# Kernel optimization log

Measured on AMD Instinct MI355X. Metric: run time of the kernel, lower is better.

Reference implementation:

```python
import jax, jax.numpy as jnp
import numpy as np

N = 100000   # nodes
E = 1600000  # edges
H = 64       # hidden_dim
NT = 512     # num_taxo
TD = 32      # taxo_dim
ID = 32      # item_dim
L = 2        # taxo_layers
ETA = 0.5
SLOPE = 0.01  # leaky_relu default


def setup_inputs() -> dict:
    key = jax.random.key(0)
    ks = jax.random.split(key, 20)
    p = lambda i, shape, s: jax.random.normal(ks[i], shape, dtype=jnp.float32) * s
    return {
        'h': p(0, (N, H), 1.0),
        'src': jax.random.randint(ks[1], (E,), 0, N),
        'dst': jax.random.randint(ks[2], (E,), 0, N),
        'taxo_cats': jax.random.randint(ks[3], (N, L), 0, NT),
        'idx_rows': jnp.arange(N),
        'idx_cols': jax.random.randint(ks[4], (N,), 0, N),
        'idx_vals': jax.random.uniform(ks[5], (N,), dtype=jnp.float32),
        'norm_rows': jnp.arange(N),
        'norm_cols': jax.random.randint(ks[6], (N,), 0, N),
        'norm_vals': jax.random.uniform(ks[7], (N,), dtype=jnp.float32),
        'W_w': p(8, (H, H), H ** -0.5),
        'W_b': jnp.zeros((H,), jnp.float32),
        'prelu_a': jnp.full((1,), 0.25, jnp.float32),
        'taxo_mean': p(9, (NT, H), 0.1),
        'taxo_std_log': p(10, (NT, H), 0.1),
        'conv_wh': p(11, (1, 2 * H), (2 * H) ** -0.5),
        'conv_Ww': p(12, (H, H), H ** -0.5),
        'conv_Wb': jnp.zeros((H,), jnp.float32),
        'psi_W': p(13, (1, H, H), H ** -0.5),
        'psi_b': jnp.zeros((1,), jnp.float32),
        'mlp_w0': p(14, (TD, H), H ** -0.5),
        'mlp_b0': jnp.zeros((TD,), jnp.float32),
        'mlp_w1': p(15, (TD, H), H ** -0.5),
        'mlp_b1': jnp.zeros((TD,), jnp.float32),
        'mlp_w2': p(16, (ID, H), H ** -0.5),
        'mlp_b2': jnp.zeros((ID,), jnp.float32),
    }


def _spmm(rows, cols, vals, x, nrows):
    # sparse COO [nrows, n] @ dense [n, d]
    return jax.ops.segment_sum(vals[:, None] * x[cols], rows, num_segments=nrows)


def _edge_softmax(scores, dst, n):
    # softmax of edge scores grouped by destination node
    m = jax.ops.segment_max(scores, dst, num_segments=n)
    e = jnp.exp(scores - m[dst])
    s = jax.ops.segment_sum(e, dst, num_segments=n)
    return e / s[dst]


def _prelu(x, a):
    return jnp.where(x >= 0, x, a * x)


def _normalize(x):
    return x / jnp.maximum(jnp.linalg.norm(x, axis=1, keepdims=True), 1e-12)


def _conv(h, tax, src, dst, wh, Ww, Wb):
    hs = h[src]  # [E,H]
    wf = jnp.concatenate([hs, h[dst]], axis=1) @ wh.T  # [E,1]
    wf = jnp.where(wf >= 0, wf, SLOPE * wf)
    alpha_f = _edge_softmax(wf, dst, N)
    wt = jnp.sum(tax[src] * tax[dst], axis=1, keepdims=True)  # [E,1]
    alpha_t = _edge_softmax(wt, dst, N)
    alpha = ETA * alpha_f + (1.0 - ETA) * alpha_t
    z = jax.ops.segment_sum(hs * alpha, dst, num_segments=N)  # u_mul_e + sum
    return z @ Ww.T + Wb


def reference(h, src, dst, taxo_cats, idx_rows, idx_cols, idx_vals,
              norm_rows, norm_cols, norm_vals, W_w, W_b, prelu_a,
              taxo_mean, taxo_std_log, conv_wh, conv_Ww, conv_Wb,
              psi_W, psi_b, mlp_w0, mlp_b0, mlp_w1, mlp_b1, mlp_w2, mlp_b2):
    h = _prelu(h @ W_w.T + W_b, prelu_a)
    means = taxo_mean[taxo_cats]            # [N,L,H]
    stds = jnp.exp(taxo_std_log[taxo_cats])  # [N,L,H]
    tax = _spmm(norm_rows, norm_cols, norm_vals, means.reshape(N, L * H), N)
    # conv layers share the SAME weights (ModuleList([ConvLayer]*num_layer))
    for i in range(2):
        h = _conv(h, tax, src, dst, conv_wh, conv_Ww, conv_Wb)
        if i < 1:
            h = _prelu(h, prelu_a)
    raw = h
    emb_h = _normalize(h @ mlp_w2.T + mlp_b2)
    embs = []
    for i, (w, b) in enumerate([(mlp_w0, mlp_b0), (mlp_w1, mlp_b1)]):
        h_rev = _spmm(idx_rows, idx_cols, idx_vals, h, N)
        mi = means[:, i]
        si = stds[:, i]
        stpl = jnp.einsum('bi,ij,bj->b', h_rev, psi_W[0], mi)[:, None] + psi_b
        tau = jax.nn.sigmoid(stpl) * jnp.exp(-si)
        cur = (1.0 - tau) * h_rev + tau * mi
        cur = _spmm(norm_rows, norm_cols, norm_vals, cur, N)
        embs.append(_normalize(cur @ w.T + b))
    emb = jnp.stack(embs, axis=2).reshape(N, -1)
    emb = jnp.concatenate([emb_h, emb], axis=1)  # [N, out_dim]
    return raw, emb
```

## Files before the change

kernel.cpp:

```cpp
#include <hip/hip_runtime.h>

constexpr int H  = 64;
constexpr int NT = 512;
constexpr int NBMAX = 512;

#define FMA4(acc_, s_, v_) { (acc_).x += (s_)*(v_).x; (acc_).y += (s_)*(v_).y; \
                             (acc_).z += (s_)*(v_).z; (acc_).w += (s_)*(v_).w; }

__global__ void k_gram(const float* __restrict__ tm, float* __restrict__ G) {
    int idx = blockIdx.x * blockDim.x + threadIdx.x;
    if (idx >= NT * NT) return;
    int a = idx >> 9, b = idx & (NT - 1);
    const float* ra = tm + a * H;
    const float* rb = tm + b * H;
    float s = 0.f;
#pragma unroll
    for (int k = 0; k < H; ++k) s += ra[k] * rb[k];
    G[idx] = s;
}

__global__ void k_nm(const int* __restrict__ ncols, const int* __restrict__ cats,
                     const float* __restrict__ nvals, uint2* __restrict__ nm, int N) {
    int n = blockIdx.x * blockDim.x + threadIdx.x;
    if (n >= N) return;
    int j = ncols[n];
    nm[n] = make_uint2(__float_as_uint(nvals[n]),
                       (unsigned)(cats[j * 2] | (cats[j * 2 + 1] << 16)));
}

__global__ void k_phist(const int* __restrict__ dst, int* __restrict__ histT,
                        int NB, int NPB, int CH, int E) {
    __shared__ int hist[NBMAX];
    int b = blockIdx.x, t = threadIdx.x;
    for (int i = t; i < NB; i += 256) hist[i] = 0;
    __syncthreads();
    int e0 = b * CH, e1 = min(E, e0 + CH);
    for (int e = e0 + t; e < e1; e += 256)
        atomicAdd(&hist[dst[e] >> 8], 1);
    __syncthreads();
    for (int i = t; i < NB; i += 256) histT[i * NPB + b] = hist[i];
}

__global__ void k_btot(const int* __restrict__ histT, int* __restrict__ tot, int NPB) {
    __shared__ int sh[256];
    int bk = blockIdx.x, t = threadIdx.x;
    int s = 0;
    for (int j = t; j < NPB; j += 256) s += histT[bk * NPB + j];
    sh[t] = s;
    __syncthreads();
    for (int o = 128; o; o >>= 1) { if (t < o) sh[t] += sh[t + o]; __syncthreads(); }
    if (!t) tot[bk] = sh[0];
}

__global__ void k_bscan(const int* __restrict__ tot, int* __restrict__ bbase,
                        int* __restrict__ row_start, int NB, int N, int E) {
    __shared__ int sh[NBMAX];
    int t = threadIdx.x;
    int v = (t < NB) ? tot[t] : 0;
    sh[t] = v;
    __syncthreads();
    for (int o = 1; o < NBMAX; o <<= 1) {
        int x = (t >= o) ? sh[t - o] : 0;
        __syncthreads();
        sh[t] += x;
        __syncthreads();
    }
    if (t < NB) bbase[t] = sh[t] - v;
    if (t == 0) { bbase[NB] = E; row_start[N] = E; }
}

__global__ void k_boff(const int* __restrict__ histT, const int* __restrict__ bbase,
                       int* __restrict__ boff, int NPB) {
    __shared__ int sh[NBMAX];
    int bk = blockIdx.x, t = threadIdx.x;
    int v = (t < NPB) ? histT[bk * NPB + t] : 0;
    sh[t] = v;
    __syncthreads();
    for (int o = 1; o < NBMAX; o <<= 1) {
        int x = (t >= o) ? sh[t - o] : 0;
        __syncthreads();
        sh[t] += x;
        __syncthreads();
    }
    if (t < NPB) boff[bk * NPB + t] = bbase[bk] + sh[t] - v;
}

__global__ void k_part(const int* __restrict__ src, const int* __restrict__ dst,
                       const int* __restrict__ boff, unsigned* __restrict__ brec,
                       int NB, int NPB, int CH, int E) {
    __shared__ int cur[NBMAX];
    int b = blockIdx.x, t = threadIdx.x;
    for (int i = t; i < NB; i += 256) cur[i] = boff[i * NPB + b];
    __syncthreads();
    int e0 = b * CH, e1 = min(E, e0 + CH);
    for (int e = e0 + t; e < e1; e += 256) {
        int s = src[e], d = dst[e];
        int pos = atomicAdd(&cur[d >> 8], 1);
        brec[pos] = (unsigned)s | ((unsigned)(d & 255) << 24);
    }
}

__global__ void k_csr(const unsigned* __restrict__ brec, const int* __restrict__ bbase,
                      const uint2* __restrict__ nm, const float* __restrict__ G,
                      int* __restrict__ row_start, int* __restrict__ src_s,
                      float* __restrict__ et, float* __restrict__ sumt, int N) {
    __shared__ int   sdeg[256];
    __shared__ int   scur[256];
    __shared__ float ssum[256];
    __shared__ float snv[256];
    __shared__ int   scc[256];
    int b = blockIdx.x, t = threadIdx.x;
    int node0 = b << 8;
    int ebase = bbase[b], eend = bbase[b + 1];
    sdeg[t] = 0; scur[t] = 0; ssum[t] = 0.f;
    int n = node0 + t;
    if (n < N) { uint2 m = nm[n]; snv[t] = __uint_as_float(m.x); scc[t] = (int)m.y; }
    __syncthreads();
    for (int i = ebase + t; i < eend; i += 256)
        atomicAdd(&sdeg[brec[i] >> 24], 1);
    __syncthreads();
    int val = sdeg[t];
    for (int o = 1; o < 256; o <<= 1) {
        int x = (t >= o) ? sdeg[t - o] : 0;
        __syncthreads();
        sdeg[t] += x;
        __syncthreads();
    }
    int gstart = ebase + sdeg[t] - val;
    if (n < N) row_start[n] = gstart;
    sdeg[t] = gstart;
    __syncthreads();
    for (int i = ebase + t; i < eend; i += 256) {
        unsigned r = brec[i];
        int s = (int)(r & 0xFFFFFFu);
        int j = (int)(r >> 24);
        int c = atomicAdd(&scur[j], 1);
        int k = sdeg[j] + c;
        src_s[k] = s;
        uint2 ms = nm[s];
        float nvs = __uint_as_float(ms.x);
        int cs = (int)ms.y;
        int cd = scc[j];
        float wt = nvs * snv[j] *
                   (G[(cs & 0xffff) * NT + (cd & 0xffff)] + G[(cs >> 16) * NT + (cd >> 16)]);
        float ev = __expf(wt);
        et[k] = ev;
        atomicAdd(&ssum[j], ev);
    }
    __syncthreads();
    if (n < N) sumt[n] = ssum[t];
}

__global__ void k_agg(const float* __restrict__ h_in, const int* __restrict__ src_s,
                      const int* __restrict__ row_start, const float* __restrict__ et,
                      const float* __restrict__ sumt, const float* __restrict__ s_u,
                      const float* __restrict__ s_v, float* __restrict__ z_out, int N) {
    int t = threadIdx.x;
    int sg = t >> 4, l16 = t & 15, f = l16 * 4;
    int n = blockIdx.x * 16 + sg;
    if (n >= N) return;
    int kb = row_start[n], ke = row_start[n + 1];
    float4 z = make_float4(0.f, 0.f, 0.f, 0.f);
    if (ke > kb) {
        float sv = s_v[n];
        float ss = 0.f;
        for (int k = kb + l16; k < ke; k += 16) {
            float w = s_u[src_s[k]] + sv;
            w = w >= 0.f ? w : 0.01f * w;
            ss += __expf(w);
        }
        ss += __shfl_xor(ss, 1); ss += __shfl_xor(ss, 2);
        ss += __shfl_xor(ss, 4); ss += __shfl_xor(ss, 8);
        float invf = 0.5f / ss;
        float invt = 0.5f / sumt[n];
        int kl = ke - 1;
        float4 z0 = make_float4(0.f, 0.f, 0.f, 0.f);
        float4 z1 = z0, z2 = z0, z3 = z0;
        for (int k0 = kb; k0 < ke; k0 += 4) {
            int kB = min(k0 + 1, kl), kC = min(k0 + 2, kl), kD = min(k0 + 3, kl);
            int sA = src_s[k0], sB = src_s[kB], sC = src_s[kC], sD = src_s[kD];
            float wA = s_u[sA] + sv; wA = wA >= 0.f ? wA : 0.01f * wA;
            float wB = s_u[sB] + sv; wB = wB >= 0.f ? wB : 0.01f * wB;
            float wC = s_u[sC] + sv; wC = wC >= 0.f ? wC : 0.01f * wC;
            float wD = s_u[sD] + sv; wD = wD >= 0.f ? wD : 0.01f * wD;
            float aA = __expf(wA) * invf + et[k0] * invt;
            float aB = (k0 + 1 <= kl) ? (__expf(wB) * invf + et[kB] * invt) : 0.f;
            float aC = (k0 + 2 <= kl) ? (__expf(wC) * invf + et[kC] * invt) : 0.f;
            float aD = (k0 + 3 <= kl) ? (__expf(wD) * invf + et[kD] * invt) : 0.f;
            const float4 hA = *reinterpret_cast<const float4*>(h_in + (size_t)sA * H + f);
            const float4 hB = *reinterpret_cast<const float4*>(h_in + (size_t)sB * H + f);
            const float4 hC = *reinterpret_cast<const float4*>(h_in + (size_t)sC * H + f);
            const float4 hD = *reinterpret_cast<const float4*>(h_in + (size_t)sD * H + f);
            FMA4(z0, aA, hA); FMA4(z1, aB, hB); FMA4(z2, aC, hC); FMA4(z3, aD, hD);
        }
        z.x = (z0.x + z1.x) + (z2.x + z3.x);
        z.y = (z0.y + z1.y) + (z2.y + z3.y);
        z.z = (z0.z + z1.z) + (z2.z + z3.z);
        z.w = (z0.w + z1.w) + (z2.w + z3.w);
    }
    *reinterpret_cast<float4*>(z_out + (size_t)n * H + f) = z;
}

template <bool PRELU, bool SUV, bool EMBH>
__global__ void __launch_bounds__(256, 4)
k_trans(const float* __restrict__ in, const float* __restrict__ W,
        const float* __restrict__ b, const float* __restrict__ a_ptr,
        const float* __restrict__ wh,
        float* __restrict__ s_u_o, float* __restrict__ s_v_o,
        const float* __restrict__ w2, const float* __restrict__ b2,
        float* __restrict__ emb_out,
        float* __restrict__ out, int N) {
    __shared__ float WF[64 * 68];
    __shared__ float W2T[EMBH ? 64 * 36 : 1];
    __shared__ float xs[4][8][68];
    int t = threadIdx.x;
    for (int i = t; i < 64 * 64; i += 256) { int j = i >> 6, l = i & 63; WF[l * 68 + j] = W[i]; }
    if constexpr (EMBH) {
        for (int i = t; i < 64 * 32; i += 256) { int j = i >> 6, l = i & 63; W2T[l * 36 + j] = w2[i]; }
    }
    __syncthreads();
    int wid = t >> 6, lane = t & 63;
    int g = lane >> 4, f = lane & 15;
    float a = PRELU ? a_ptr[0] : 0.f;
    float4 bias = *reinterpret_cast<const float4*>(b + 4 * f);
    int n0 = blockIdx.x * 32 + wid * 8 + g;
    int n1 = n0 + 4;
    float4 xv0 = make_float4(0.f, 0.f, 0.f, 0.f), xv1 = xv0;
    if (n0 < N) xv0 = *reinterpret_cast<const float4*>(in + (size_t)n0 * H + 4 * f);
    if (n1 < N) xv1 = *reinterpret_cast<const float4*>(in + (size_t)n1 * H + 4 * f);
    *reinterpret_cast<float4*>(&xs[wid][g][4 * f])     = xv0;
    *reinterpret_cast<float4*>(&xs[wid][4 + g][4 * f]) = xv1;
    float4 accP = make_float4(0.f, 0.f, 0.f, 0.f), accQ = accP;
#pragma unroll 2
    for (int l0 = 0; l0 < 64; l0 += 4) {
        const float* wp = &WF[l0 * 68 + 4 * f];
        float4 wv0 = *reinterpret_cast<const float4*>(wp);
        float4 wv1 = *reinterpret_cast<const float4*>(wp + 68);
        float4 wv2 = *reinterpret_cast<const float4*>(wp + 136);
        float4 wv3 = *reinterpret_cast<const float4*>(wp + 204);
        float4 xP = *reinterpret_cast<const float4*>(&xs[wid][g][l0]);
        float4 xQ = *reinterpret_cast<const float4*>(&xs[wid][4 + g][l0]);
        FMA4(accP, xP.x, wv0); FMA4(accP, xP.y, wv1);
        FMA4(accP, xP.z, wv2); FMA4(accP, xP.w, wv3);
        FMA4(accQ, xQ.x, wv0); FMA4(accQ, xQ.y, wv1);
        FMA4(accQ, xQ.z, wv2); FMA4(accQ, xQ.w, wv3);
    }
    auto epi = [&](float4 acc, int n, int slot) {
        acc.x += bias.x; acc.y += bias.y; acc.z += bias.z; acc.w += bias.w;
        if constexpr (PRELU) {
            acc.x = acc.x >= 0.f ? acc.x : a * acc.x;
            acc.y = acc.y >= 0.f ? acc.y : a * acc.y;
            acc.z = acc.z >= 0.f ? acc.z : a * acc.z;
            acc.w = acc.w >= 0.f ? acc.w : a * acc.w;
        }
        if (n < N) *reinterpret_cast<float4*>(out + (size_t)n * H + 4 * f) = acc;
        if constexpr (SUV) {
            float4 wu = *reinterpret_cast<const float4*>(wh + 4 * f);
            float4 wv = *reinterpret_cast<const float4*>(wh + H + 4 * f);
            float u = acc.x * wu.x + acc.y * wu.y + acc.z * wu.z + acc.w * wu.w;
            float v = acc.x * wv.x + acc.y * wv.y + acc.z * wv.z + acc.w * wv.w;
            u += __shfl_xor(u, 1); v += __shfl_xor(v, 1);
            u += __shfl_xor(u, 2); v += __shfl_xor(v, 2);
            u += __shfl_xor(u, 4); v += __shfl_xor(v, 4);
            u += __shfl_xor(u, 8); v += __shfl_xor(v, 8);
            if (f == 0 && n < N) { s_u_o[n] = u; s_v_o[n] = v; }
        }
        if constexpr (EMBH) {
            *reinterpret_cast<float4*>(&xs[wid][slot][4 * f]) = acc;
            if (f < 8) {
                float4 e4 = *reinterpret_cast<const float4*>(b2 + 4 * f);
#pragma unroll 4
                for (int l0 = 0; l0 < 64; l0 += 4) {
                    float4 x4 = *reinterpret_cast<const float4*>(&xs[wid][slot][l0]);
                    float4 u0 = *reinterpret_cast<const float4*>(&W2T[(l0 + 0) * 36 + 4 * f]);
                    float4 u1 = *reinterpret_cast<const float4*>(&W2T[(l0 + 1) * 36 + 4 * f]);
                    float4 u2 = *reinterpret_cast<const float4*>(&W2T[(l0 + 2) * 36 + 4 * f]);
                    float4 u3 = *reinterpret_cast<const float4*>(&W2T[(l0 + 3) * 36 + 4 * f]);
                    FMA4(e4, x4.x, u0); FMA4(e4, x4.y, u1);
                    FMA4(e4, x4.z, u2); FMA4(e4, x4.w, u3);
                }
                float sq = e4.x * e4.x + e4.y * e4.y + e4.z * e4.z + e4.w * e4.w;
                sq += __shfl_xor(sq, 1);
                sq += __shfl_xor(sq, 2);
                sq += __shfl_xor(sq, 4);
                float invn = 1.f / fmaxf(sqrtf(sq), 1e-12f);
                e4.x *= invn; e4.y *= invn; e4.z *= invn; e4.w *= invn;
                if (n < N) *reinterpret_cast<float4*>(emb_out + (size_t)n * 96 + 4 * f) = e4;
            }
        }
    };
    epi(accP, n0, g);
    epi(accQ, n1, 4 + g);
}

__global__ void __launch_bounds__(256, 4)
k_post1(const float* __restrict__ raw, const int* __restrict__ icols,
        const float* __restrict__ ivals, const float* __restrict__ Psi,
        const float* __restrict__ psib, const int* __restrict__ cats,
        const float* __restrict__ tm, const float* __restrict__ tsl,
        float* __restrict__ cur0, float* __restrict__ cur1, int N) {
    __shared__ float PF[64 * 68];
    __shared__ float xs[4][8][68];
    int t = threadIdx.x;
    for (int i = t; i < 64 * 64; i += 256) { int l = i >> 6, j = i & 63; PF[l * 68 + j] = Psi[i]; }
    __syncthreads();
    int wid = t >> 6, lane = t & 63;
    int g = lane >> 4, f = lane & 15;
    float pb = psib[0];
    int n0 = blockIdx.x * 32 + wid * 8 + g;
    int n1 = n0 + 4;
    float4 hr0 = make_float4(0.f, 0.f, 0.f, 0.f), hr1 = hr0;
    if (n0 < N) {
        int c = icols[n0]; float iv = ivals[n0];
        float4 rv = *reinterpret_cast<const float4*>(raw + (size_t)c * H + 4 * f);
        hr0.x = iv * rv.x; hr0.y = iv * rv.y; hr0.z = iv * rv.z; hr0.w = iv * rv.w;
    }
    if (n1 < N) {
        int c = icols[n1]; float iv = ivals[n1];
        float4 rv = *reinterpret_cast<const float4*>(raw + (size_t)c * H + 4 * f);
        hr1.x = iv * rv.x; hr1.y = iv * rv.y; hr1.z = iv * rv.z; hr1.w = iv * rv.w;
    }
    *reinterpret_cast<float4*>(&xs[wid][g][4 * f])     = hr0;
    *reinterpret_cast<float4*>(&xs[wid][4 + g][4 * f]) = hr1;
    float4 v0 = make_float4(0.f, 0.f, 0.f, 0.f), v1 = v0;
#pragma unroll 2
    for (int l0 = 0; l0 < 64; l0 += 4) {
        const float* pp = &PF[l0 * 68 + 4 * f];
        float4 pv0 = *reinterpret_cast<const float4*>(pp);
        float4 pv1 = *reinterpret_cast<const float4*>(pp + 68);
        float4 pv2 = *reinterpret_cast<const float4*>(pp + 136);
        float4 pv3 = *reinterpret_cast<const float4*>(pp + 204);
        float4 xP = *reinterpret_cast<const float4*>(&xs[wid][g][l0]);
        float4 xQ = *reinterpret_cast<const float4*>(&xs[wid][4 + g][l0]);
        FMA4(v0, xP.x, pv0); FMA4(v0, xP.y, pv1); FMA4(v0, xP.z, pv2); FMA4(v0, xP.w, pv3);
        FMA4(v1, xQ.x, pv0); FMA4(v1, xQ.y, pv1); FMA4(v1, xQ.z, pv2); FMA4(v1, xQ.w, pv3);
    }
    auto epi = [&](float4 v, float4 hr, int n) {
        if (n >= N) return;
#pragma unroll
        for (int i2 = 0; i2 < 2; ++i2) {
            int c = cats[n * 2 + i2];
            float4 m4 = *reinterpret_cast<const float4*>(tm + (size_t)c * H + 4 * f);
            float sd = v.x * m4.x + v.y * m4.y + v.z * m4.z + v.w * m4.w;
            sd += __shfl_xor(sd, 1);
            sd += __shfl_xor(sd, 2);
            sd += __shfl_xor(sd, 4);
            sd += __shfl_xor(sd, 8);
            float sig = 1.f / (1.f + __expf(-(sd + pb)));
            float4 t4 = *reinterpret_cast<const float4*>(tsl + (size_t)c * H + 4 * f);
            float4 tau, cv;
            tau.x = sig * __expf(-__expf(t4.x));
            tau.y = sig * __expf(-__expf(t4.y));
            tau.z = sig * __expf(-__expf(t4.z));
            tau.w = sig * __expf(-__expf(t4.w));
            cv.x = (1.f - tau.x) * hr.x + tau.x * m4.x;
            cv.y = (1.f - tau.y) * hr.y + tau.y * m4.y;
            cv.z = (1.f - tau.z) * hr.z + tau.z * m4.z;
            cv.w = (1.f - tau.w) * hr.w + tau.w * m4.w;
            *reinterpret_cast<float4*>((i2 ? cur1 : cur0) + (size_t)n * H + 4 * f) = cv;
        }
    };
    epi(v0, hr0, n0);
    epi(v1, hr1, n1);
}

__global__ void __launch_bounds__(256, 4)
k_post2(const float* __restrict__ cur0, const float* __restrict__ cur1,
        const int* __restrict__ ncols, const float* __restrict__ nvals,
        const float* __restrict__ w0, const float* __restrict__ b0,
        const float* __restrict__ w1, const float* __restrict__ b1,
        float* __restrict__ emb_out, int N) {
    __shared__ float WC[64 * 68];
    __shared__ float xs[4][4][2][68];
    int t = threadIdx.x;
    for (int i = t; i < 64 * 64; i += 256) {
        int j = i >> 6, l = i & 63;
        WC[l * 68 + j] = (j < 32) ? w0[j * 64 + l] : w1[(j - 32) * 64 + l];
    }
    __syncthreads();
    int wid = t >> 6, lane = t & 63;
    int g = lane >> 4, f = lane & 15;
    int half = f >> 3;
    const float* bb = half ? b1 : b0;
    float4 bias = *reinterpret_cast<const float4*>(bb + 4 * (f & 7));
    for (int it = 0; it < 2; ++it) {
        int n = blockIdx.x * 32 + wid * 8 + it * 4 + g;
        float4 x0 = make_float4(0.f, 0.f, 0.f, 0.f), x1 = x0;
        if (n < N) {
            int c = ncols[n];
            float gsc = nvals[n];
            float4 c0v = *reinterpret_cast<const float4*>(cur0 + (size_t)c * H + 4 * f);
            float4 c1v = *reinterpret_cast<const float4*>(cur1 + (size_t)c * H + 4 * f);
            x0.x = gsc * c0v.x; x0.y = gsc * c0v.y; x0.z = gsc * c0v.z; x0.w = gsc * c0v.w;
            x1.x = gsc * c1v.x; x1.y = gsc * c1v.y; x1.z = gsc * c1v.z; x1.w = gsc * c1v.w;
        }
        *reinterpret_cast<float4*>(&xs[wid][g][0][4 * f]) = x0;
        *reinterpret_cast<float4*>(&xs[wid][g][1][4 * f]) = x1;
        float4 acc = bias;
#pragma unroll 4
        for (int l0 = 0; l0 < 64; l0 += 4) {
            float4 x4  = *reinterpret_cast<const float4*>(&xs[wid][g][half][l0]);
            float4 wv0 = *reinterpret_cast<const float4*>(&WC[(l0 + 0) * 68 + 4 * f]);
            float4 wv1 = *reinterpret_cast<const float4*>(&WC[(l0 + 1) * 68 + 4 * f]);
            float4 wv2 = *reinterpret_cast<const float4*>(&WC[(l0 + 2) * 68 + 4 * f]);
            float4 wv3 = *reinterpret_cast<const float4*>(&WC[(l0 + 3) * 68 + 4 * f]);
            FMA4(acc, x4.x, wv0); FMA4(acc, x4.y, wv1);
            FMA4(acc, x4.z, wv2); FMA4(acc, x4.w, wv3);
        }
        float sq = acc.x * acc.x + acc.y * acc.y + acc.z * acc.z + acc.w * acc.w;
        sq += __shfl_xor(sq, 1);
        sq += __shfl_xor(sq, 2);
        sq += __shfl_xor(sq, 4);
        float invn = 1.f / fmaxf(sqrtf(sq), 1e-12f);
        if (n < N) {
            int jb = (f & 7) * 4;
            float* o = emb_out + (size_t)n * 96 + 32 + half;
            o[2 * (jb + 0)] = acc.x * invn;
            o[2 * (jb + 1)] = acc.y * invn;
            o[2 * (jb + 2)] = acc.z * invn;
            o[2 * (jb + 3)] = acc.w * invn;
        }
    }
}

extern "C" void kernel_launch(void* const* d_in, const int* in_sizes, int n_in,
                              void* d_out, int out_size, void* d_ws, size_t ws_size,
                              hipStream_t stream) {
    const float* h      = (const float*)d_in[0];
    const int*   src    = (const int*)d_in[1];
    const int*   dst    = (const int*)d_in[2];
    const int*   cats   = (const int*)d_in[3];
    const int*   icols  = (const int*)d_in[5];
    const float* ivals  = (const float*)d_in[6];
    const int*   ncols  = (const int*)d_in[8];
    const float* nvals  = (const float*)d_in[9];
    const float* W_w    = (const float*)d_in[10];
    const float* W_b    = (const float*)d_in[11];
    const float* pre_a  = (const float*)d_in[12];
    const float* tm     = (const float*)d_in[13];
    const float* tsl    = (const float*)d_in[14];
    const float* wh     = (const float*)d_in[15];
    const float* cWw    = (const float*)d_in[16];
    const float* cWb    = (const float*)d_in[17];
    const float* psiW   = (const float*)d_in[18];
    const float* psib   = (const float*)d_in[19];
    const float* w0     = (const float*)d_in[20];
    const float* b0     = (const float*)d_in[21];
    const float* w1     = (const float*)d_in[22];
    const float* b1     = (const float*)d_in[23];
    const float* w2     = (const float*)d_in[24];
    const float* b2     = (const float*)d_in[25];

    const int N = in_sizes[0] / H;
    const int E = in_sizes[1];
    const int NB = (N + 255) >> 8;
    const int NPB = NB;
    const int CH = (E + NPB - 1) / NPB;

    char* ws = (char*)d_ws;
    size_t off = 0;
    auto alloc = [&](size_t bytes) -> void* {
        void* p = ws + off;
        off = (off + bytes + 255) & ~(size_t)255;
        return p;
    };
    float*    A        = (float*)   alloc((size_t)N * H * 4);
    float*    B        = (float*)   alloc((size_t)N * H * 4);
    float*    Z        = (float*)   alloc((size_t)N * H * 4);
    float*    et       = (float*)   alloc((size_t)E * 4);
    int*      src_s    = (int*)     alloc((size_t)E * 4);
    unsigned* brec     = (unsigned*)alloc((size_t)E * 4);
    uint2*    nm       = (uint2*)   alloc((size_t)N * 8);
    int*      row_start= (int*)     alloc((size_t)(N + 1) * 4);
    float*    sumt     = (float*)   alloc((size_t)N * 4);
    float*    s_u0     = (float*)   alloc((size_t)N * 4);
    float*    s_v0     = (float*)   alloc((size_t)N * 4);
    float*    s_u1     = (float*)   alloc((size_t)N * 4);
    float*    s_v1     = (float*)   alloc((size_t)N * 4);
    float*    G        = (float*)   alloc((size_t)NT * NT * 4);
    int*      histT    = (int*)     alloc((size_t)NB * NPB * 4);
    int*      boff     = (int*)     alloc((size_t)NB * NPB * 4);
    int*      tot      = (int*)     alloc((size_t)NB * 4);
    int*      bbase    = (int*)     alloc((size_t)(NB + 1) * 4);
    (void)ws_size; (void)n_in; (void)out_size;

    float* rawOut  = (float*)d_out;
    float* emb_out = (float*)d_out + (size_t)N * H;

    dim3 b256(256);
    int nb16 = (N + 15) / 16;
    int nb32 = (N + 31) / 32;

    k_gram<<<(NT * NT + 255) / 256, b256, 0, stream>>>(tm, G);
    k_nm<<<(N + 255) / 256, b256, 0, stream>>>(ncols, cats, nvals, nm, N);
    k_phist<<<NPB, b256, 0, stream>>>(dst, histT, NB, NPB, CH, E);
    k_btot<<<NB, b256, 0, stream>>>(histT, tot, NPB);
    k_bscan<<<1, NBMAX, 0, stream>>>(tot, bbase, row_start, NB, N, E);
    k_boff<<<NB, NBMAX, 0, stream>>>(histT, bbase, boff, NPB);
    k_part<<<NPB, b256, 0, stream>>>(src, dst, boff, brec, NB, NPB, CH, E);
    k_csr<<<NB, b256, 0, stream>>>(brec, bbase, nm, G, row_start, src_s, et, sumt, N);

    k_trans<true, true, false><<<nb32, b256, 0, stream>>>(
        h, W_w, W_b, pre_a, wh, s_u0, s_v0, nullptr, nullptr, nullptr, A, N);

    k_agg<<<nb16, b256, 0, stream>>>(A, src_s, row_start, et, sumt, s_u0, s_v0, Z, N);
    k_trans<true, true, false><<<nb32, b256, 0, stream>>>(
        Z, cWw, cWb, pre_a, wh, s_u1, s_v1, nullptr, nullptr, nullptr, B, N);

    k_agg<<<nb16, b256, 0, stream>>>(B, src_s, row_start, et, sumt, s_u1, s_v1, Z, N);
    k_trans<false, false, true><<<nb32, b256, 0, stream>>>(
        Z, cWw, cWb, pre_a, nullptr, nullptr, nullptr, w2, b2, emb_out, rawOut, N);

    k_post1<<<nb32, b256, 0, stream>>>(rawOut, icols, ivals, psiW, psib, cats, tm, tsl,
                                       A, B, N);
    k_post2<<<nb32, b256, 0, stream>>>(A, B, ncols, nvals, w0, b0, w1, b1, emb_out, N);
}
```

Before: 373.0 us.

## Split edge-weight computation into separate kernel and shuffle-broadcast indices in aggregation

Moves the per-edge attention weight computation (leaky-relu, exp, normalisation by both softmax sums) out of k_agg into a new one-thread-per-node kernel k_ef that writes alpha into the reused brec buffer. k_agg then loads 16 edge indices and weights cooperatively per sub-group and broadcasts them with __shfl, so the 16 lanes no longer each perform redundant scalar loads and exp work for every edge. This adds an extra kernel launch per layer plus an E-sized write and read of alpha. The k_ef kernel walks each node's edges serially, twice, in a single thread, and its memory accesses are poorly coalesced.

```diff
diff --git a/kernel.cpp b/kernel.cpp
--- a/kernel.cpp
+++ b/kernel.cpp
@@ -151,53 +151,70 @@
     if (n < N) sumt[n] = ssum[t];
 }
 
+__global__ void k_ef(const int* __restrict__ src_s, const int* __restrict__ row_start,
+                     const float* __restrict__ et, const float* __restrict__ sumt,
+                     const float* __restrict__ s_u, const float* __restrict__ s_v,
+                     float* __restrict__ alpha, int N) {
+    int n = blockIdx.x * blockDim.x + threadIdx.x;
+    if (n >= N) return;
+    int kb = row_start[n], ke = row_start[n + 1];
+    if (ke <= kb) return;
+    float sv = s_v[n];
+    float ssf = 0.f;
+    for (int k = kb; k < ke; ++k) {
+        float w = s_u[src_s[k]] + sv;
+        w = w >= 0.f ? w : 0.01f * w;
+        ssf += __expf(w);
+    }
+    float invf = 0.5f / ssf;
+    float invt = 0.5f / sumt[n];
+    for (int k = kb; k < ke; ++k) {
+        float w = s_u[src_s[k]] + sv;
+        w = w >= 0.f ? w : 0.01f * w;
+        alpha[k] = __expf(w) * invf + et[k] * invt;
+    }
+}
+
 __global__ void k_agg(const float* __restrict__ h_in, const int* __restrict__ src_s,
-                      const int* __restrict__ row_start, const float* __restrict__ et,
-                      const float* __restrict__ sumt, const float* __restrict__ s_u,
-                      const float* __restrict__ s_v, float* __restrict__ z_out, int N) {
+                      const int* __restrict__ row_start, const float* __restrict__ alpha,
+                      float* __restrict__ z_out, int N) {
     int t = threadIdx.x;
     int sg = t >> 4, l16 = t & 15, f = l16 * 4;
     int n = blockIdx.x * 16 + sg;
     if (n >= N) return;
     int kb = row_start[n], ke = row_start[n + 1];
-    float4 z = make_float4(0.f, 0.f, 0.f, 0.f);
-    if (ke > kb) {
-        float sv = s_v[n];
-        float ss = 0.f;
-        for (int k = kb + l16; k < ke; k += 16) {
-            float w = s_u[src_s[k]] + sv;
-            w = w >= 0.f ? w : 0.01f * w;
-            ss += __expf(w);
-        }
-        ss += __shfl_xor(ss, 1); ss += __shfl_xor(ss, 2);
-        ss += __shfl_xor(ss, 4); ss += __shfl_xor(ss, 8);
-        float invf = 0.5f / ss;
-        float invt = 0.5f / sumt[n];
-        int kl = ke - 1;
-        float4 z0 = make_float4(0.f, 0.f, 0.f, 0.f);
-        float4 z1 = z0, z2 = z0, z3 = z0;
-        for (int k0 = kb; k0 < ke; k0 += 4) {
-            int kB = min(k0 + 1, kl), kC = min(k0 + 2, kl), kD = min(k0 + 3, kl);
-            int sA = src_s[k0], sB = src_s[kB], sC = src_s[kC], sD = src_s[kD];
-            float wA = s_u[sA] + sv; wA = wA >= 0.f ? wA : 0.01f * wA;
-            float wB = s_u[sB] + sv; wB = wB >= 0.f ? wB : 0.01f * wB;
-            float wC = s_u[sC] + sv; wC = wC >= 0.f ? wC : 0.01f * wC;
-            float wD = s_u[sD] + sv; wD = wD >= 0.f ? wD : 0.01f * wD;
-            float aA = __expf(wA) * invf + et[k0] * invt;
-            float aB = (k0 + 1 <= kl) ? (__expf(wB) * invf + et[kB] * invt) : 0.f;
-            float aC = (k0 + 2 <= kl) ? (__expf(wC) * invf + et[kC] * invt) : 0.f;
-            float aD = (k0 + 3 <= kl) ? (__expf(wD) * invf + et[kD] * invt) : 0.f;
+    float4 z0 = make_float4(0.f, 0.f, 0.f, 0.f);
+    float4 z1 = z0, z2 = z0, z3 = z0;
+    for (int k0 = kb; k0 < ke; k0 += 16) {
+        int cnt = ke - k0; cnt = cnt < 16 ? cnt : 16;
+        int cl = cnt - 1;
+        int myk = k0 + (l16 <= cl ? l16 : cl);
+        int ms = src_s[myk];
+        float ma = (l16 <= cl) ? alpha[myk] : 0.f;
+        for (int j0 = 0; j0 < cnt; j0 += 4) {
+            int jB = min(j0 + 1, cl), jC = min(j0 + 2, cl), jD = min(j0 + 3, cl);
+            int sA = __shfl(ms, j0, 16), sB = __shfl(ms, jB, 16);
+            int sC = __shfl(ms, jC, 16), sD = __shfl(ms, jD, 16);
+            float taA = __shfl(ma, j0, 16), taB = __shfl(ma, jB, 16);
+            float taC = __shfl(ma, jC, 16), taD = __shfl(ma, jD, 16);
+            float aB = (j0 + 1 <= cl) ? taB : 0.f;
+            float aC = (j0 + 2 <= cl) ? taC : 0.f;
+            float aD = (j0 + 3 <= cl) ? taD : 0.f;
             const float4 hA = *reinterpret_cast<const float4*>(h_in + (size_t)sA * H + f);
             const float4 hB = *reinterpret_cast<const float4*>(h_in + (size_t)sB * H + f);
             const float4 hC = *reinterpret_cast<const float4*>(h_in + (size_t)sC * H + f);
             const float4 hD = *reinterpret_cast<const float4*>(h_in + (size_t)sD * H + f);
-            FMA4(z0, aA, hA); FMA4(z1, aB, hB); FMA4(z2, aC, hC); FMA4(z3, aD, hD);
-        }
-        z.x = (z0.x + z1.x) + (z2.x + z3.x);
-        z.y = (z0.y + z1.y) + (z2.y + z3.y);
-        z.z = (z0.z + z1.z) + (z2.z + z3.z);
-        z.w = (z0.w + z1.w) + (z2.w + z3.w);
-    }
+            FMA4(z0, taA, hA);
+            FMA4(z1, aB, hB);
+            FMA4(z2, aC, hC);
+            FMA4(z3, aD, hD);
+        }
+    }
+    float4 z;
+    z.x = (z0.x + z1.x) + (z2.x + z3.x);
+    z.y = (z0.y + z1.y) + (z2.y + z3.y);
+    z.z = (z0.z + z1.z) + (z2.z + z3.z);
+    z.w = (z0.w + z1.w) + (z2.w + z3.w);
     *reinterpret_cast<float4*>(z_out + (size_t)n * H + f) = z;
 }
 
@@ -484,15 +501,18 @@
     int*      bbase    = (int*)     alloc((size_t)(NB + 1) * 4);
     (void)ws_size; (void)n_in; (void)out_size;
 
+    float* alpha = (float*)brec;
+
     float* rawOut  = (float*)d_out;
     float* emb_out = (float*)d_out + (size_t)N * H;
 
     dim3 b256(256);
     int nb16 = (N + 15) / 16;
     int nb32 = (N + 31) / 32;
+    int nbN  = (N + 255) / 256;
 
     k_gram<<<(NT * NT + 255) / 256, b256, 0, stream>>>(tm, G);
-    k_nm<<<(N + 255) / 256, b256, 0, stream>>>(ncols, cats, nvals, nm, N);
+    k_nm<<<nbN, b256, 0, stream>>>(ncols, cats, nvals, nm, N);
     k_phist<<<NPB, b256, 0, stream>>>(dst, histT, NB, NPB, CH, E);
     k_btot<<<NB, b256, 0, stream>>>(histT, tot, NPB);
     k_bscan<<<1, NBMAX, 0, stream>>>(tot, bbase, row_start, NB, N, E);
@@ -503,11 +523,13 @@
     k_trans<true, true, false><<<nb32, b256, 0, stream>>>(
         h, W_w, W_b, pre_a, wh, s_u0, s_v0, nullptr, nullptr, nullptr, A, N);
 
-    k_agg<<<nb16, b256, 0, stream>>>(A, src_s, row_start, et, sumt, s_u0, s_v0, Z, N);
+    k_ef<<<nbN, b256, 0, stream>>>(src_s, row_start, et, sumt, s_u0, s_v0, alpha, N);
+    k_agg<<<nb16, b256, 0, stream>>>(A, src_s, row_start, alpha, Z, N);
     k_trans<true, true, false><<<nb32, b256, 0, stream>>>(
         Z, cWw, cWb, pre_a, wh, s_u1, s_v1, nullptr, nullptr, nullptr, B, N);
 
-    k_agg<<<nb16, b256, 0, stream>>>(B, src_s, row_start, et, sumt, s_u1, s_v1, Z, N);
+    k_ef<<<nbN, b256, 0, stream>>>(src_s, row_start, et, sumt, s_u1, s_v1, alpha, N);
+    k_agg<<<nb16, b256, 0, stream>>>(B, src_s, row_start, alpha, Z, N);
     k_trans<false, false, true><<<nb32, b256, 0, stream>>>(
         Z, cWw, cWb, pre_a, nullptr, nullptr, nullptr, w2, b2, emb_out, rawOut, N);
 
```

Result: slower. 421.5 us (+13.0%).
